# Kernel tuning notes

Hardware: AMD Instinct MI355X
Metric: run time of the kernel (lower is better)

## Reference

```python
import jax, jax.numpy as jnp
import numpy as np

B, T, C = 1, 2048, 2048
N_HEADS, N_KV_HEADS = 32, 8
D_HEAD = C // N_HEADS  # 64
WINDOW = 512
ROPE_BASE = 10000.0


def setup_inputs() -> dict:
    key = jax.random.key(0)
    ks = jax.random.split(key, 5)
    s = 0.02
    return {
        "x": jax.random.normal(ks[0], (B, T, C), dtype=jnp.float32),
        "wq": jax.random.normal(ks[1], (C, N_HEADS * D_HEAD), dtype=jnp.float32) * s,
        "wk": jax.random.normal(ks[2], (C, N_KV_HEADS * D_HEAD), dtype=jnp.float32) * s,
        "wv": jax.random.normal(ks[3], (C, N_KV_HEADS * D_HEAD), dtype=jnp.float32) * s,
        "wo": jax.random.normal(ks[4], (N_HEADS * D_HEAD, C), dtype=jnp.float32) * s,
    }


def _rope_tables(seq_len, d_head, dtype):
    inv_freq = 1.0 / (ROPE_BASE ** (jnp.arange(0, d_head, 2, dtype=jnp.float32) / d_head))
    t = jnp.arange(seq_len, dtype=jnp.float32)
    freqs = t[:, None] * inv_freq[None, :]          # [T, d/2]
    emb = jnp.concatenate([freqs, freqs], axis=-1)  # [T, d]
    return jnp.cos(emb).astype(dtype), jnp.sin(emb).astype(dtype)


def _rotate_half(u):
    d = u.shape[-1]
    return jnp.concatenate([-u[..., d // 2:], u[..., :d // 2]], axis=-1)


def reference(x, wq, wk, wv, wo):
    b, t, c = x.shape
    n_rep = N_HEADS // N_KV_HEADS
    q = (x @ wq).reshape(b, t, N_HEADS, D_HEAD)
    k = (x @ wk).reshape(b, t, N_KV_HEADS, D_HEAD)
    v = (x @ wv).reshape(b, t, N_KV_HEADS, D_HEAD)

    cos, sin = _rope_tables(t, D_HEAD, x.dtype)
    cos = cos[None, :, None, :]
    sin = sin[None, :, None, :]
    q = q * cos + _rotate_half(q) * sin
    k = k * cos + _rotate_half(k) * sin

    # repeat_interleave KV heads up to n_heads (GQA expansion)
    k = jnp.repeat(k, n_rep, axis=2)  # [B,T,H,d]
    v = jnp.repeat(v, n_rep, axis=2)

    scale = 1.0 / np.sqrt(D_HEAD)
    scores = jnp.einsum('bqhd,bkhd->bhqk', q, k) * scale  # [B,H,T,T]

    # sliding-window causal mask: attend iff k<=q and q-k<=window
    qi = jnp.arange(t)[:, None]
    ki = jnp.arange(t)[None, :]
    allowed = (ki <= qi) & (qi - ki <= WINDOW)  # [T,T] bool
    scores = jnp.where(allowed[None, None, :, :], scores, -jnp.inf)

    attn = jax.nn.softmax(scores, axis=-1)
    out = jnp.einsum('bhqk,bkhd->bqhd', attn, v).reshape(b, t, N_HEADS * D_HEAD)
    return out @ wo
```

## Files before the change

### kernel.cpp

```cpp
#include <hip/hip_runtime.h>
#include <hip/hip_bf16.h>
#include <math.h>

#define T_SEQ 2048
#define C_DIM 2048
#define NH    32
#define NKV   8
#define DH    64
#define WIN   512
#define QKV_N 3072

typedef __bf16 bf16x8 __attribute__((ext_vector_type(8)));
typedef __bf16 bf16x4 __attribute__((ext_vector_type(4)));
typedef float  f32x4  __attribute__((ext_vector_type(4)));

#if __has_builtin(__builtin_amdgcn_exp2f)
#define EXP2(x) __builtin_amdgcn_exp2f(x)
#else
#define EXP2(x) exp2f(x)
#endif

__device__ __forceinline__ void gload_lds16(const __bf16* g, __bf16* l) {
  __builtin_amdgcn_global_load_lds(
      (const __attribute__((address_space(1))) void*)g,
      (__attribute__((address_space(3))) void*)l, 16, 0, 0);
}

__device__ __forceinline__ void tr_tile(const float* __restrict__ in,
                                        __bf16* __restrict__ out,
                                        int R, int Ccols, int tile, int tid,
                                        float (*sh)[33]) {
  int tpc = Ccols >> 5;
  int c0 = (tile % tpc) << 5;
  int r0 = (tile / tpc) << 5;
  int tx = tid & 31, ty = tid >> 5;
#pragma unroll
  for (int i = 0; i < 32; i += 8)
    sh[ty + i][tx] = in[(size_t)(r0 + ty + i) * Ccols + c0 + tx];
  __syncthreads();
#pragma unroll
  for (int i = 0; i < 32; i += 8)
    out[(size_t)(c0 + ty + i) * R + r0 + tx] = (__bf16)sh[tx][ty + i];
}

__global__ __launch_bounds__(256) void prep_kernel(
    const float* __restrict__ x, const float* __restrict__ wq,
    const float* __restrict__ wk, const float* __restrict__ wv,
    __bf16* __restrict__ xb, __bf16* __restrict__ wqkvT,
    float2* __restrict__ tab) {
  __shared__ float sh[32][33];
  int bid = blockIdx.x;
  const int tid = threadIdx.x;
  if (bid < 4096) {
    int i = bid * 256 + tid;
    float4 v = ((const float4*)x)[i];
    bf16x4 o = {(__bf16)v.x, (__bf16)v.y, (__bf16)v.z, (__bf16)v.w};
    *(bf16x4*)(xb + (size_t)i * 4) = o;
    return;
  }
  bid -= 4096;
  if (bid < 256) {
    int i = bid * 256 + tid;
    int j = i & 31, t = i >> 5;
    float inv = powf(10000.0f, -(float)(2 * j) / 64.0f);
    float s, c;
    sincosf((float)t * inv, &s, &c);
    tab[i] = make_float2(c, s);
    return;
  }
  bid -= 256;
  if (bid < 4096) { tr_tile(wq, wqkvT, C_DIM, C_DIM, bid, tid, sh); return; }
  bid -= 4096;
  if (bid < 1024) {
    tr_tile(wk, wqkvT + (size_t)2048 * C_DIM, C_DIM, NKV * DH, bid, tid, sh);
    return;
  }
  bid -= 1024;
  tr_tile(wv, wqkvT + (size_t)2560 * C_DIM, C_DIM, NKV * DH, bid, tid, sh);
}

template <typename OutT, bool ROPE>
__global__ __launch_bounds__(512) void gemm_bf16_kernel(
    const __bf16* __restrict__ A, const __bf16* __restrict__ Bt,
    OutT* __restrict__ C, const float2* __restrict__ rope_tab,
    int M, int N, int K, int chx, int chy) {
  __shared__ __bf16 As[2][128 * 64];
  __shared__ __bf16 Bs[2][64 * 64];

  const int tid = threadIdx.x;
  const int wid = tid >> 6, l = tid & 63;
  const int lm = l & 15, lh = l >> 4;

  const int hw  = blockIdx.x;
  const int xcd = hw & 7;
  const int idx = hw >> 3;
  const int bx  = (xcd & 3) * chx + idx % chx;
  const int by  = (xcd >> 2) * chy + idx / chx;
  const int brow = by * 128, bcol = bx * 64;

  const int kb_swz = (((l & 7) ^ (l >> 3)) << 3);
  const int srow   = l >> 3;

  auto stage = [&](int kbase, int bi) {
#pragma unroll
    for (int c = 0; c < 3; ++c) {
      int ci = wid + c * 8;
      if (ci < 16) {
        int row = ci * 8 + srow;
        gload_lds16(A + (size_t)(brow + row) * K + kbase + kb_swz,
                    &As[bi][ci * 512]);
      } else {
        int row = (ci - 16) * 8 + srow;
        gload_lds16(Bt + (size_t)(bcol + row) * K + kbase + kb_swz,
                    &Bs[bi][(ci - 16) * 512]);
      }
    }
  };

  f32x4 acc[4] = {};
  const int NT = K >> 6;

  stage(0, 0);
  __syncthreads();

  for (int t = 0; t < NT; ++t) {
    const int cur = t & 1;
    if (t + 1 < NT) stage((t + 1) << 6, cur ^ 1);

    const __bf16* as = As[cur];
    const __bf16* bs = Bs[cur];
    const int x7 = lm & 7;
    bf16x8 af[2], bfr[4][2];
#pragma unroll
    for (int u = 0; u < 2; ++u)
      af[u] = *(const bf16x8*)&as[(wid * 16 + lm) * 64 +
                                  (((u * 4 + lh) ^ x7) << 3)];
#pragma unroll
    for (int j = 0; j < 4; ++j)
#pragma unroll
      for (int u = 0; u < 2; ++u)
        bfr[j][u] = *(const bf16x8*)&bs[(j * 16 + lm) * 64 +
                                        (((u * 4 + lh) ^ x7) << 3)];
#pragma unroll
    for (int u = 0; u < 2; ++u)
#pragma unroll
      for (int j = 0; j < 4; ++j)
        acc[j] = __builtin_amdgcn_mfma_f32_16x16x32_bf16(
            af[u], bfr[j][u], acc[j], 0, 0, 0);

    __syncthreads();
  }

  if (ROPE) {
    if (bcol < 2560) {
#pragma unroll
      for (int r = 0; r < 4; ++r) {
        int t = brow + wid * 16 + lh * 4 + r;
#pragma unroll
        for (int j = 0; j < 2; ++j) {
          float2 cs = rope_tab[t * 32 + j * 16 + lm];
          float v0 = acc[j][r], v1 = acc[j + 2][r];
          acc[j][r]     = v0 * cs.x - v1 * cs.y;
          acc[j + 2][r] = v1 * cs.x + v0 * cs.y;
        }
      }
    }
    if (bcol < 2048) {
#pragma unroll
      for (int j = 0; j < 4; ++j)
#pragma unroll
        for (int r = 0; r < 4; ++r) acc[j][r] *= 0.18033688f;
    }
  }

#pragma unroll
  for (int j = 0; j < 4; ++j)
#pragma unroll
    for (int r = 0; r < 4; ++r) {
      int row = brow + wid * 16 + lh * 4 + r;
      int col = bcol + j * 16 + lm;
      C[(size_t)row * N + col] = (OutT)acc[j][r];
    }
}

__global__ __launch_bounds__(256) void attn_mfma_kernel(
    const __bf16* __restrict__ QKV, __bf16* __restrict__ O,
    const float* __restrict__ wo, __bf16* __restrict__ woT) {
  const int tid = threadIdx.x;

  if (blockIdx.x >= 1024) {
    __shared__ float sh[32][33];
    tr_tile(wo, woT, C_DIM, C_DIM, blockIdx.x - 1024, tid, sh);
    return;
  }

  __shared__ __bf16 K_lds[64][72];
  __shared__ __bf16 Vt[64][72];
  __shared__ __bf16 P_lds[4][16][72];

  const int l   = tid & 63;
  const int w   = tid >> 6;
  const int q0  = (blockIdx.x & 31) * 64;
  const int h   = blockIdx.x >> 5;
  const int kvh = h >> 2;
  const int q0w = q0 + w * 16;
  const int lm  = l & 15;
  const int lh  = l >> 4;

  const __bf16* Qp = QKV + h * DH;
  const __bf16* Kp = QKV + 2048 + kvh * DH;
  const __bf16* Vp = QKV + 2560 + kvh * DH;

  bf16x8 aq0 = *(const bf16x8*)(Qp + (size_t)(q0w + lm) * QKV_N + lh * 8);
  bf16x8 aq1 = *(const bf16x8*)(Qp + (size_t)(q0w + lm) * QKV_N + 32 + lh * 8);

  f32x4 o_acc[4] = {};
  float m = -60.0f, lsum = 0.0f;

  const int klo  = (q0 - WIN) > 0 ? (q0 - WIN) : 0;
  const int skey = tid >> 2;
  const int sdp  = (tid & 3) * 16;

  for (int k0 = klo; k0 < q0 + 64; k0 += 64) {
    __syncthreads();
    {
      const __bf16* ks = Kp + (size_t)(k0 + skey) * QKV_N + sdp;
      *(bf16x8*)&K_lds[skey][sdp]     = *(const bf16x8*)ks;
      *(bf16x8*)&K_lds[skey][sdp + 8] = *(const bf16x8*)(ks + 8);
      const __bf16* vs = Vp + (size_t)(k0 + l) * QKV_N + w * 16;
      bf16x8 v0 = *(const bf16x8*)vs;
      bf16x8 v1 = *(const bf16x8*)(vs + 8);
#pragma unroll
      for (int j = 0; j < 8; ++j) Vt[w * 16 + j][l]     = v0[j];
#pragma unroll
      for (int j = 0; j < 8; ++j) Vt[w * 16 + 8 + j][l] = v1[j];
    }
    __syncthreads();

    f32x4 s[4] = {};
#pragma unroll
    for (int kg = 0; kg < 4; ++kg) {
      bf16x8 kb0 = *(const bf16x8*)&K_lds[kg * 16 + lm][lh * 8];
      bf16x8 kb1 = *(const bf16x8*)&K_lds[kg * 16 + lm][32 + lh * 8];
      s[kg] = __builtin_amdgcn_mfma_f32_16x16x32_bf16(kb0, aq0, s[kg], 0, 0, 0);
      s[kg] = __builtin_amdgcn_mfma_f32_16x16x32_bf16(kb1, aq1, s[kg], 0, 0, 0);
    }

    float sv[4][4];
    const bool full = (k0 + 63 <= q0w) && (k0 >= q0w + 15 - WIN);
    if (full) {
#pragma unroll
      for (int kg = 0; kg < 4; ++kg)
#pragma unroll
        for (int r = 0; r < 4; ++r) sv[kg][r] = s[kg][r];
    } else {
      const int qr = q0w + lm;
#pragma unroll
      for (int kg = 0; kg < 4; ++kg)
#pragma unroll
        for (int r = 0; r < 4; ++r) {
          int kc = k0 + kg * 16 + lh * 4 + r;
          sv[kg][r] = (kc <= qr && kc + WIN >= qr) ? s[kg][r] : -1e30f;
        }
    }

    float t01 = fmaxf(fmaxf(fmaxf(sv[0][0], sv[0][1]), fmaxf(sv[0][2], sv[0][3])),
                      fmaxf(fmaxf(sv[1][0], sv[1][1]), fmaxf(sv[1][2], sv[1][3])));
    float t23 = fmaxf(fmaxf(fmaxf(sv[2][0], sv[2][1]), fmaxf(sv[2][2], sv[2][3])),
                      fmaxf(fmaxf(sv[3][0], sv[3][1]), fmaxf(sv[3][2], sv[3][3])));
    float tmax = fmaxf(t01, t23);
    tmax = fmaxf(tmax, __shfl_xor(tmax, 16));
    tmax = fmaxf(tmax, __shfl_xor(tmax, 32));

    float mn = fmaxf(m, tmax);
    float co = EXP2(m - mn);
    m = mn;
    float ps = 0.0f;
#pragma unroll
    for (int kg = 0; kg < 4; ++kg)
#pragma unroll
      for (int r = 0; r < 4; ++r) {
        float p = EXP2(sv[kg][r] - mn);
        sv[kg][r] = p;
        ps += p;
      }
    ps += __shfl_xor(ps, 16);
    ps += __shfl_xor(ps, 32);
    lsum = lsum * co + ps;
#pragma unroll
    for (int dc = 0; dc < 4; ++dc)
#pragma unroll
      for (int r = 0; r < 4; ++r) o_acc[dc][r] *= co;

#pragma unroll
    for (int kg = 0; kg < 4; ++kg)
#pragma unroll
      for (int r = 0; r < 4; ++r)
        P_lds[w][lm][kg * 16 + lh * 4 + r] = (__bf16)sv[kg][r];
    bf16x8 pf0 = *(const bf16x8*)&P_lds[w][lm][lh * 8];
    bf16x8 pf1 = *(const bf16x8*)&P_lds[w][lm][32 + lh * 8];

#pragma unroll
    for (int dc = 0; dc < 4; ++dc) {
      bf16x8 vb0 = *(const bf16x8*)&Vt[dc * 16 + lm][lh * 8];
      bf16x8 vb1 = *(const bf16x8*)&Vt[dc * 16 + lm][32 + lh * 8];
      o_acc[dc] = __builtin_amdgcn_mfma_f32_16x16x32_bf16(vb0, pf0, o_acc[dc], 0, 0, 0);
      o_acc[dc] = __builtin_amdgcn_mfma_f32_16x16x32_bf16(vb1, pf1, o_acc[dc], 0, 0, 0);
    }
  }

  const float inv = 1.0f / lsum;
#pragma unroll
  for (int dc = 0; dc < 4; ++dc) {
    bf16x4 ov;
#pragma unroll
    for (int r = 0; r < 4; ++r) ov[r] = (__bf16)(o_acc[dc][r] * inv);
    *(bf16x4*)&O[(size_t)(q0w + lm) * C_DIM + h * DH + dc * 16 + lh * 4] = ov;
  }
}

extern "C" void kernel_launch(void* const* d_in, const int* in_sizes, int n_in,
                              void* d_out, int out_size, void* d_ws, size_t ws_size,
                              hipStream_t stream) {
  const float* x  = (const float*)d_in[0];
  const float* wq = (const float*)d_in[1];
  const float* wk = (const float*)d_in[2];
  const float* wv = (const float*)d_in[3];
  const float* wo = (const float*)d_in[4];
  float* out = (float*)d_out;

  __bf16* xb    = (__bf16*)d_ws;
  __bf16* wqkvT = xb + (size_t)C_DIM * C_DIM;
  __bf16* woT   = wqkvT + (size_t)QKV_N * C_DIM;
  __bf16* QKV   = woT + (size_t)C_DIM * C_DIM;
  float2* tab   = (float2*)(QKV + (size_t)T_SEQ * QKV_N);
  __bf16* Ab    = xb;

  prep_kernel<<<4096 + 256 + 4096 + 1024 + 1024, 256, 0, stream>>>(
      x, wq, wk, wv, xb, wqkvT, tab);

  gemm_bf16_kernel<__bf16, true>
      <<<768, 512, 0, stream>>>(
          xb, wqkvT, QKV, tab, T_SEQ, QKV_N, C_DIM, 12, 8);

  attn_mfma_kernel<<<1024 + 4096, 256, 0, stream>>>(QKV, Ab, wo, woT);

  gemm_bf16_kernel<float, false>
      <<<512, 512, 0, stream>>>(
          Ab, woT, out, nullptr, T_SEQ, C_DIM, C_DIM, 8, 8);
}
```

Before: 108.2 us.

## Use 128x128 tiles with 32x32x16 MFMA for the fused QKV projection GEMM

```diff
diff --git a/kernel.cpp b/kernel.cpp
--- a/kernel.cpp
+++ b/kernel.cpp
@@ -13,6 +13,7 @@
 typedef __bf16 bf16x8 __attribute__((ext_vector_type(8)));
 typedef __bf16 bf16x4 __attribute__((ext_vector_type(4)));
 typedef float  f32x4  __attribute__((ext_vector_type(4)));
+typedef float  f32x16 __attribute__((ext_vector_type(16)));
 
 #if __has_builtin(__builtin_amdgcn_exp2f)
 #define EXP2(x) __builtin_amdgcn_exp2f(x)
@@ -80,10 +81,111 @@
 }
 
 template <typename OutT, bool ROPE>
-__global__ __launch_bounds__(512) void gemm_bf16_kernel(
+__global__ __launch_bounds__(256) void gemm32_bf16_kernel(
     const __bf16* __restrict__ A, const __bf16* __restrict__ Bt,
     OutT* __restrict__ C, const float2* __restrict__ rope_tab,
     int M, int N, int K, int chx, int chy) {
+  __shared__ __bf16 As[2][128 * 64];
+  __shared__ __bf16 Bs[2][128 * 64];
+
+  const int tid = threadIdx.x;
+  const int wid = tid >> 6, l = tid & 63;
+  const int wr = wid >> 1, wc = wid & 1;
+  const int l31 = l & 31, lhi = l >> 5;
+
+  const int hw  = blockIdx.x;
+  const int xcd = hw & 7;
+  const int idx = hw >> 3;
+  const int bx  = (xcd & 3) * chx + idx % chx;
+  const int by  = (xcd >> 2) * chy + idx / chx;
+  const int brow = by * 128, bcol = bx * 128;
+
+  const int kb_swz = (((l & 7) ^ (l >> 3)) << 3);
+  const int srow   = l >> 3;
+
+  auto stage = [&](int kbase, int bi) {
+#pragma unroll
+    for (int c = 0; c < 8; ++c) {
+      int ci = wid + c * 4;
+      if (ci < 16) {
+        int row = ci * 8 + srow;
+        gload_lds16(A + (size_t)(brow + row) * K + kbase + kb_swz,
+                    &As[bi][ci * 512]);
+      } else {
+        int row = (ci - 16) * 8 + srow;
+        gload_lds16(Bt + (size_t)(bcol + row) * K + kbase + kb_swz,
+                    &Bs[bi][(ci - 16) * 512]);
+      }
+    }
+  };
+
+  f32x16 acc[2][2] = {};
+  const int NT = K >> 6;
+
+  stage(0, 0);
+  __syncthreads();
+
+  const int x7 = l & 7;
+  for (int t = 0; t < NT; ++t) {
+    const int cur = t & 1;
+    if (t + 1 < NT) stage((t + 1) << 6, cur ^ 1);
+
+    const __bf16* as = As[cur];
+    const __bf16* bs = Bs[cur];
+#pragma unroll
+    for (int kc = 0; kc < 4; ++kc) {
+      const int ko = (((kc * 2 + lhi) ^ x7) << 3);
+      bf16x8 a0 = *(const bf16x8*)&as[(wr * 64 + l31) * 64 + ko];
+      bf16x8 a1 = *(const bf16x8*)&as[(wr * 64 + 32 + l31) * 64 + ko];
+      bf16x8 b0 = *(const bf16x8*)&bs[(wc * 64 + l31) * 64 + ko];
+      bf16x8 b1 = *(const bf16x8*)&bs[(wc * 64 + 32 + l31) * 64 + ko];
+      acc[0][0] = __builtin_amdgcn_mfma_f32_32x32x16_bf16(a0, b0, acc[0][0], 0, 0, 0);
+      acc[0][1] = __builtin_amdgcn_mfma_f32_32x32x16_bf16(a0, b1, acc[0][1], 0, 0, 0);
+      acc[1][0] = __builtin_amdgcn_mfma_f32_32x32x16_bf16(a1, b0, acc[1][0], 0, 0, 0);
+      acc[1][1] = __builtin_amdgcn_mfma_f32_32x32x16_bf16(a1, b1, acc[1][1], 0, 0, 0);
+    }
+    __syncthreads();
+  }
+
+  if (ROPE) {
+    if (bcol < 2560) {
+#pragma unroll
+      for (int i = 0; i < 2; ++i)
+#pragma unroll
+        for (int r = 0; r < 16; ++r) {
+          int trow = brow + wr * 64 + i * 32 + (r & 3) + 8 * (r >> 2) + 4 * lhi;
+          float2 cs = rope_tab[trow * 32 + l31];
+          float v0 = acc[i][0][r], v1 = acc[i][1][r];
+          acc[i][0][r] = v0 * cs.x - v1 * cs.y;
+          acc[i][1][r] = v1 * cs.x + v0 * cs.y;
+        }
+    }
+    if (bcol < 2048) {
+#pragma unroll
+      for (int i = 0; i < 2; ++i)
+#pragma unroll
+        for (int j = 0; j < 2; ++j)
+#pragma unroll
+          for (int r = 0; r < 16; ++r) acc[i][j][r] *= 0.18033688f;
+    }
+  }
+
+#pragma unroll
+  for (int i = 0; i < 2; ++i)
+#pragma unroll
+    for (int j = 0; j < 2; ++j)
+#pragma unroll
+      for (int r = 0; r < 16; ++r) {
+        int row = brow + wr * 64 + i * 32 + (r & 3) + 8 * (r >> 2) + 4 * lhi;
+        int col = bcol + wc * 64 + j * 32 + l31;
+        C[(size_t)row * N + col] = (OutT)acc[i][j][r];
+      }
+}
+
+template <typename OutT>
+__global__ __launch_bounds__(512) void gemm_bf16_kernel(
+    const __bf16* __restrict__ A, const __bf16* __restrict__ Bt,
+    OutT* __restrict__ C, int M, int N, int K, int chx, int chy) {
   __shared__ __bf16 As[2][128 * 64];
   __shared__ __bf16 Bs[2][64 * 64];
 
@@ -151,28 +253,6 @@
     __syncthreads();
   }
 
-  if (ROPE) {
-    if (bcol < 2560) {
-#pragma unroll
-      for (int r = 0; r < 4; ++r) {
-        int t = brow + wid * 16 + lh * 4 + r;
-#pragma unroll
-        for (int j = 0; j < 2; ++j) {
-          float2 cs = rope_tab[t * 32 + j * 16 + lm];
-          float v0 = acc[j][r], v1 = acc[j + 2][r];
-          acc[j][r]     = v0 * cs.x - v1 * cs.y;
-          acc[j + 2][r] = v1 * cs.x + v0 * cs.y;
-        }
-      }
-    }
-    if (bcol < 2048) {
-#pragma unroll
-      for (int j = 0; j < 4; ++j)
-#pragma unroll
-        for (int r = 0; r < 4; ++r) acc[j][r] *= 0.18033688f;
-    }
-  }
-
 #pragma unroll
   for (int j = 0; j < 4; ++j)
 #pragma unroll
@@ -339,13 +419,13 @@
   prep_kernel<<<4096 + 256 + 4096 + 1024 + 1024, 256, 0, stream>>>(
       x, wq, wk, wv, xb, wqkvT, tab);
 
-  gemm_bf16_kernel<__bf16, true>
-      <<<768, 512, 0, stream>>>(
-          xb, wqkvT, QKV, tab, T_SEQ, QKV_N, C_DIM, 12, 8);
+  gemm32_bf16_kernel<__bf16, true>
+      <<<384, 256, 0, stream>>>(
+          xb, wqkvT, QKV, tab, T_SEQ, QKV_N, C_DIM, 6, 8);
 
   attn_mfma_kernel<<<1024 + 4096, 256, 0, stream>>>(QKV, Ab, wo, woT);
 
-  gemm_bf16_kernel<float, false>
+  gemm_bf16_kernel<float>
       <<<512, 512, 0, stream>>>(
-          Ab, woT, out, nullptr, T_SEQ, C_DIM, C_DIM, 8, 8);
-}
+          Ab, woT, out, T_SEQ, C_DIM, C_DIM, 8, 8);
+}
```

New measurement: 111.9 us (median of 2 runs). 1.03x slower.
